# Kernel optimization log

Hardware: AMD Instinct MI355X
Metric: run time of the kernel (lower is better)

The kernel has to match this reference:

```python
import jax, jax.numpy as jnp
import numpy as np

SHIFT_MAX = 20.0  # max |offset| in pixels; padded margin is (M-N)/2 = 32

def setup_inputs() -> dict:
    key = jax.random.key(0)
    k1, k2 = jax.random.split(key)
    B, M, N, C = 2048, 128, 64, 4
    padded_obj = jax.random.normal(k1, (B, M, M, 1), dtype=jnp.float32)
    # channel-format offsets (B,1,2,C): [...,0,:] = x (col) shift, [...,1,:] = y (row) shift
    positions = (jax.random.uniform(k2, (B, 1, 2, C), dtype=jnp.float32) - 0.5) * 2.0 * SHIFT_MAX
    return {"padded_obj": padded_obj, "positions": positions, "N": N}


def _bilinear_extract(padded_obj, positions, N):
    # padded_obj: (B,M,M,1), positions: (B,1,2,C) -> patches (B,N,N,C)
    # Equivalent to: translate each (per-channel) copy of the object by -offset
    # with bilinear interpolation and zero fill, then crop the central NxN.
    B, M = padded_obj.shape[0], padded_obj.shape[1]
    C = positions.shape[-1]
    img = padded_obj[..., 0]                       # (B,M,M)
    ox = positions[:, 0, 0, :]                     # (B,C) x (column) offset
    oy = positions[:, 0, 1, :]                     # (B,C) y (row) offset
    c0 = (M - N) // 2                              # crop origin
    r = jnp.arange(N, dtype=positions.dtype)
    # sample coordinates in source image: out(r,c) = img(r + c0 + oy, c + c0 + ox)
    yy = r[None, None, :] + c0 + oy[..., None]     # (B,C,N)
    xx = r[None, None, :] + c0 + ox[..., None]     # (B,C,N)
    y0 = jnp.floor(yy)
    x0 = jnp.floor(xx)
    wy = (yy - y0)[:, :, :, None]                  # (B,C,N,1) row frac
    wx = (xx - x0)[:, :, None, :]                  # (B,C,1,N) col frac
    y0i = y0.astype(jnp.int32)
    x0i = x0.astype(jnp.int32)
    b_idx = jnp.arange(B)[:, None, None, None]

    def gather(yi, xi):
        # yi: (B,C,N) rows, xi: (B,C,N) cols -> (B,C,N,N) with zero fill OOB
        valid = ((yi[:, :, :, None] >= 0) & (yi[:, :, :, None] < M)
                 & (xi[:, :, None, :] >= 0) & (xi[:, :, None, :] < M))
        yc = jnp.clip(yi, 0, M - 1)[:, :, :, None]
        xc = jnp.clip(xi, 0, M - 1)[:, :, None, :]
        vals = img[b_idx, yc, xc]                  # (B,C,N,N)
        return jnp.where(valid, vals, jnp.zeros((), vals.dtype))

    v00 = gather(y0i, x0i)
    v01 = gather(y0i, x0i + 1)
    v10 = gather(y0i + 1, x0i)
    v11 = gather(y0i + 1, x0i + 1)
    patch = (v00 * (1 - wy) * (1 - wx) + v01 * (1 - wy) * wx
             + v10 * wy * (1 - wx) + v11 * wy * wx)   # (B,C,N,N)
    return jnp.transpose(patch, (0, 2, 3, 1))          # (B,N,N,C)


def reference(padded_obj, positions, N):
    return _bilinear_extract(padded_obj, positions, N)
```

## Files before the change

kernel.cpp:

```cpp
#include <hip/hip_runtime.h>


constexpr int Mdim   = 128;
constexpr int Npatch = 64;
constexpr int Cc     = 4;
constexpr int C0     = 32;

__global__ __launch_bounds__(256) void extract_patches_kernel(
    const float* __restrict__ img,
    const float* __restrict__ pos,
    float* __restrict__ out)
{
    const int b = blockIdx.x;
    const float* __restrict__ imgb = img + (size_t)b * (Mdim * Mdim);
    const float* __restrict__ pb   = pos + (size_t)b * (2 * Cc);

    float w00[Cc], w01[Cc], w10[Cc], w11[Cc];
    int   ixv[Cc], iyv[Cc];
#pragma unroll
    for (int c = 0; c < Cc; ++c) {
        const float ox = pb[c];
        const float oy = pb[Cc + c];
        const float fx = floorf(ox);
        const float fy = floorf(oy);
        const float wx = ox - fx;
        const float wy = oy - fy;
        ixv[c] = C0 + (int)fx;
        iyv[c] = C0 + (int)fy;
        w00[c] = (1.0f - wy) * (1.0f - wx);
        w01[c] = (1.0f - wy) * wx;
        w10[c] = wy * (1.0f - wx);
        w11[c] = wy * wx;
    }

    const int tid = threadIdx.x;
    const int j  = tid & (Npatch - 1);
    const int i0 = tid >> 6;

    for (int i = i0; i < Npatch; i += 4) {
        float4 o;
        float* res = reinterpret_cast<float*>(&o);
#pragma unroll
        for (int c = 0; c < Cc; ++c) {
            const float* p = imgb + (iyv[c] + i) * Mdim + ixv[c] + j;
            const float v00 = p[0];
            const float v01 = p[1];
            const float v10 = p[Mdim];
            const float v11 = p[Mdim + 1];
            res[c] = w00[c] * v00 + w01[c] * v01 + w10[c] * v10 + w11[c] * v11;
        }
        float4* optr = reinterpret_cast<float4*>(
            out + (((size_t)b * Npatch + i) * Npatch + j) * Cc);
        *optr = o;
    }
}

extern "C" void kernel_launch(void* const* d_in, const int* in_sizes, int n_in,
                              void* d_out, int out_size, void* d_ws, size_t ws_size,
                              hipStream_t stream) {
    const float* img = (const float*)d_in[0];
    const float* pos = (const float*)d_in[1];
    float* out = (float*)d_out;

    const int B = in_sizes[0] / (Mdim * Mdim);
    extract_patches_kernel<<<dim3(B), dim3(256), 0, stream>>>(img, pos, out);
}
```

Baseline: 253.7 us.

## Stage reachable image rows into LDS via async global_load_lds, use 512 threads

Each block copies rows 12..115 of its image (the only rows reachable with shifts up to 20 px) into shared memory using direct global-to-LDS loads, then does the four-tap bilinear reads from LDS instead of global memory/L2. The block size doubles to 512 threads so more waves take part in the copy and the output loop. It trades redundant global gathers for a roughly 53 KB LDS footprint per block, which limits how many blocks fit per CU, and adds a barrier. It also relies on offsets staying within the assumed row window.

```diff
diff --git a/kernel.cpp b/kernel.cpp
--- a/kernel.cpp
+++ b/kernel.cpp
@@ -5,18 +5,35 @@
 constexpr int Npatch = 64;
 constexpr int Cc     = 4;
 constexpr int C0     = 32;
+constexpr int ROW0   = 12;
+constexpr int NROWS  = 104;
 
-__global__ __launch_bounds__(256) void extract_patches_kernel(
+__global__ __launch_bounds__(512) void extract_patches_kernel(
     const float* __restrict__ img,
     const float* __restrict__ pos,
     float* __restrict__ out)
 {
+    __shared__ float lds[NROWS * Mdim];
+
     const int b = blockIdx.x;
     const float* __restrict__ imgb = img + (size_t)b * (Mdim * Mdim);
     const float* __restrict__ pb   = pos + (size_t)b * (2 * Cc);
 
+    const int tid  = threadIdx.x;
+    const int lane = tid & 63;
+    const int wave = tid >> 6;
+
+    const float* src = imgb + ROW0 * Mdim;
+    for (int w = wave; w < (NROWS * Mdim) / 256; w += 8) {
+        const float* g = src + w * 256 + lane * 4;
+        __builtin_amdgcn_global_load_lds(
+            (const __attribute__((address_space(1))) void*)g,
+            (__attribute__((address_space(3))) void*)&lds[w * 256],
+            16, 0, 0);
+    }
+
     float w00[Cc], w01[Cc], w10[Cc], w11[Cc];
-    int   ixv[Cc], iyv[Cc];
+    int   base0[Cc];
 #pragma unroll
     for (int c = 0; c < Cc; ++c) {
         const float ox = pb[c];
@@ -25,28 +42,30 @@
         const float fy = floorf(oy);
         const float wx = ox - fx;
         const float wy = oy - fy;
-        ixv[c] = C0 + (int)fx;
-        iyv[c] = C0 + (int)fy;
+        const int ix = C0 + (int)fx;
+        const int iy = C0 + (int)fy;
+        base0[c] = (iy - ROW0) * Mdim + ix;
         w00[c] = (1.0f - wy) * (1.0f - wx);
         w01[c] = (1.0f - wy) * wx;
         w10[c] = wy * (1.0f - wx);
         w11[c] = wy * wx;
     }
 
-    const int tid = threadIdx.x;
+    __syncthreads();
+
     const int j  = tid & (Npatch - 1);
     const int i0 = tid >> 6;
 
-    for (int i = i0; i < Npatch; i += 4) {
+    for (int i = i0; i < Npatch; i += 8) {
         float4 o;
         float* res = reinterpret_cast<float*>(&o);
 #pragma unroll
         for (int c = 0; c < Cc; ++c) {
-            const float* p = imgb + (iyv[c] + i) * Mdim + ixv[c] + j;
-            const float v00 = p[0];
-            const float v01 = p[1];
-            const float v10 = p[Mdim];
-            const float v11 = p[Mdim + 1];
+            const int base = base0[c] + i * Mdim + j;
+            const float v00 = lds[base];
+            const float v01 = lds[base + 1];
+            const float v10 = lds[base + Mdim];
+            const float v11 = lds[base + Mdim + 1];
             res[c] = w00[c] * v00 + w01[c] * v01 + w10[c] * v10 + w11[c] * v11;
         }
         float4* optr = reinterpret_cast<float4*>(
@@ -63,5 +82,5 @@
     float* out = (float*)d_out;
 
     const int B = in_sizes[0] / (Mdim * Mdim);
-    extract_patches_kernel<<<dim3(B), dim3(256), 0, stream>>>(img, pos, out);
+    extract_patches_kernel<<<dim3(B), dim3(512), 0, stream>>>(img, pos, out);
 }
```

Result: faster. 232.4 us (-8.4%).
